# Performance work log

Measured on AMD Instinct MI355X. Metric: run time of the kernel, lower is better.

## Reference

```python
import jax, jax.numpy as jnp
import numpy as np

H = 128      # num_hidden
C = 384      # num_in
K = 32       # neighbors
N = 10000    # nodes
SCALE = 30.0
EPS = 1e-5

def _gelu(x):
    return jax.nn.gelu(x, approximate=False)  # torch GELU default is exact erf

def _ln(x, g, b):
    m = jnp.mean(x, axis=-1, keepdims=True)
    v = jnp.mean((x - m) ** 2, axis=-1, keepdims=True)
    return (x - m) * jax.lax.rsqrt(v + EPS) * g + b

def setup_inputs() -> dict:
    key = jax.random.key(0)
    ks = jax.random.split(key, 12)
    s = lambda fan_in: 1.0 / np.sqrt(fan_in)
    # weights stored [in, out] (transposed vs torch nn.Linear)
    return {
        "h_V": jax.random.normal(ks[0], (N, H), jnp.float32),
        "h_E": jax.random.normal(ks[1], (N, K, C), jnp.float32),
        "mask_V": jnp.ones((N,), jnp.float32),
        "mask_attend": jnp.ones((N, K), jnp.float32),
        "W1_w": jax.random.uniform(ks[2], (H + C, H), jnp.float32, -s(H + C), s(H + C)),
        "W1_b": jnp.zeros((H,), jnp.float32),
        "W2_w": jax.random.uniform(ks[3], (H, H), jnp.float32, -s(H), s(H)),
        "W2_b": jnp.zeros((H,), jnp.float32),
        "W3_w": jax.random.uniform(ks[4], (H, H), jnp.float32, -s(H), s(H)),
        "W3_b": jnp.zeros((H,), jnp.float32),
        "ln1_g": jnp.ones((H,), jnp.float32),
        "ln1_b": jnp.zeros((H,), jnp.float32),
        "Win_w": jax.random.uniform(ks[5], (H, 4 * H), jnp.float32, -s(H), s(H)),
        "Win_b": jnp.zeros((4 * H,), jnp.float32),
        "Wout_w": jax.random.uniform(ks[6], (4 * H, H), jnp.float32, -s(4 * H), s(4 * H)),
        "Wout_b": jnp.zeros((H,), jnp.float32),
        "ln2_g": jnp.ones((H,), jnp.float32),
        "ln2_b": jnp.zeros((H,), jnp.float32),
    }

def reference(h_V, h_E, mask_V, mask_attend,
              W1_w, W1_b, W2_w, W2_b, W3_w, W3_b,
              ln1_g, ln1_b, Win_w, Win_b, Wout_w, Wout_b, ln2_g, ln2_b):
    # expand node features along neighbor axis and concat with edge features
    h_V_expand = jnp.broadcast_to(h_V[:, None, :], (h_V.shape[0], h_E.shape[1], h_V.shape[1]))
    h_EV = jnp.concatenate([h_V_expand, h_E], axis=-1)          # [N, K, H+C]
    # per-edge 3-layer MLP message
    h = _gelu(h_EV @ W1_w + W1_b)                               # [N, K, H]
    h = _gelu(h @ W2_w + W2_b)
    h_message = h @ W3_w + W3_b
    h_message = mask_attend[..., None] * h_message
    dh = jnp.sum(h_message, axis=-2) / SCALE                    # [N, H]
    h_V = _ln(h_V + dh, ln1_g, ln1_b)
    # position-wise FFN
    dh = _gelu(h_V @ Win_w + Win_b) @ Wout_w + Wout_b
    h_V = _ln(h_V + dh, ln2_g, ln2_b)
    h_V = mask_V[:, None] * h_V
    return h_V
```

## Files before the change

### kernel.cpp

```cpp
#include <hip/hip_runtime.h>
#include <hip/hip_bf16.h>

#define NH 128
#define NC 384
#define NK 32

typedef __attribute__((ext_vector_type(8))) short short8v;
typedef __attribute__((ext_vector_type(4))) float f32x4;

#define MFMA16(a, b, c) __builtin_amdgcn_mfma_f32_16x16x32_bf16((a), (b), (c), 0, 0, 0)

__device__ __forceinline__ ushort f2bf(float x) {
  __hip_bfloat16 h = __float2bfloat16(x);
  ushort u;
  __builtin_memcpy(&u, &h, 2);
  return u;
}

__device__ __forceinline__ short8v ld8(const ushort* p) {
  return *reinterpret_cast<const short8v*>(p);
}
__device__ __forceinline__ void st8(ushort* p, short8v v) {
  *reinterpret_cast<short8v*>(p) = v;
}

__device__ __forceinline__ short8v pack8(float4 a, float4 b) {
  short8v v;
  v[0] = (short)f2bf(a.x); v[1] = (short)f2bf(a.y);
  v[2] = (short)f2bf(a.z); v[3] = (short)f2bf(a.w);
  v[4] = (short)f2bf(b.x); v[5] = (short)f2bf(b.y);
  v[6] = (short)f2bf(b.z); v[7] = (short)f2bf(b.w);
  return v;
}

__device__ __forceinline__ float gelu_f(float x) {
  float x2 = x * x;
  float m = __builtin_fmaf(0.07135481283f, x2, 1.595769122f);
  float e = __expf(-x * m);
  return x * __builtin_amdgcn_rcpf(1.0f + e);
}

__device__ __forceinline__ void gload_lds16(const float* g, float* l) {
  __builtin_amdgcn_global_load_lds(
      (const __attribute__((address_space(1))) unsigned int*)g,
      (__attribute__((address_space(3))) unsigned int*)l, 16, 0, 0);
}

__global__ __launch_bounds__(256) void pack_w(
    const float* __restrict__ W1, const float* __restrict__ W2,
    const float* __restrict__ W3, const float* __restrict__ Win,
    const float* __restrict__ Wout, ushort* __restrict__ ws) {
  int id = blockIdx.x * 256 + threadIdx.x;
  if (id < 65536) {
    int t = id, k = t >> 7, c = t & 127;
    ws[(((k >> 3) << 7) + c) * 8 + (k & 7)] = f2bf(W1[t]);
  } else if (id < 81920) {
    int t = id - 65536, k = t >> 7, c = t & 127;
    ws[65536 + (((k >> 3) << 7) + c) * 8 + (k & 7)] = f2bf(W2[t]);
  } else if (id < 98304) {
    int t = id - 81920, k = t >> 7, c = t & 127;
    ws[81920 + (((k >> 3) << 7) + c) * 8 + (k & 7)] = f2bf(W3[t]);
  } else if (id < 163840) {
    int t = id - 98304, k = t >> 9, c = t & 511;
    ws[98304 + (((k >> 3) << 9) + c) * 8 + (k & 7)] = f2bf(Win[t]);
  } else {
    int t = id - 163840, k = t >> 7, c = t & 127;
    ws[163840 + (((k >> 3) << 7) + c) * 8 + (k & 7)] = f2bf(Wout[t]);
  }
}


__device__ __forceinline__ void stage_issue(const float* __restrict__ hE,
    float* sF, int p, int chunk, int tid, int N) {
  const int w = tid >> 6, l = tid & 63;
#pragma unroll
  for (int j = 0; j < 4; ++j) {
    const int base16 = j * 512 + w * 64;
    const int fidx = (base16 + l) * 4;
    const int row = fidx >> 7;
    const int col = fidx & 127;
    const int node = row >> 5, e = row & 31;
    int n = 2 * p + node;
    if (n >= N) n = 0;
    const float* g = hE + ((size_t)n * NK + e) * NC + chunk * 128 + col;
    gload_lds16(g, sF + base16 * 4);
  }
}

__device__ __forceinline__ void convert_chunk(const float* sF, ushort* sB, int tid) {
#pragma unroll
  for (int j = 0; j < 4; ++j) {
    const int fi = j * 2048 + tid * 4;
    const float4 v = *reinterpret_cast<const float4*>(sF + fi);
    const int row = fi >> 7;
    const int col = fi & 127;
    const int c8 = col >> 3;
    ushort4 o;
    o.x = f2bf(v.x); o.y = f2bf(v.y); o.z = f2bf(v.z); o.w = f2bf(v.w);
    *reinterpret_cast<ushort4*>(sB + row * 128 + ((c8 ^ (row & 15)) << 3) + (col & 7)) = o;
  }
}

__device__ __forceinline__ void mfma_chunk(const ushort* __restrict__ buf,
    const ushort* __restrict__ Wp, int ktBase, f32x4 acc[4],
    int g, int lr, int colbase) {
#pragma unroll
  for (int j = 0; j < 4; ++j) {
    short8v b = ld8(Wp + (((ktBase + j) * 4 + g) * 128 + colbase) * 8);
    const int kcg = j * 4 + g;
#pragma unroll
    for (int rt = 0; rt < 4; ++rt) {
      const int row = rt * 16 + lr;
      short8v a = ld8(buf + row * 128 + ((kcg ^ (row & 15)) << 3));
      acc[rt] = MFMA16(a, b, acc[rt]);
    }
  }
}

__device__ __forceinline__ void epi_store(ushort* __restrict__ buf,
    const f32x4 acc[4], const float* __restrict__ bias, int colbase, int g) {
  const float bs = bias[colbase];
#pragma unroll
  for (int rt = 0; rt < 4; ++rt)
#pragma unroll
    for (int i = 0; i < 4; ++i) {
      const int rr = rt * 16 + g * 4 + i;
      buf[rr * 128 + ((((colbase >> 3) ^ (rr & 15)) << 3) | (colbase & 7))] =
          f2bf(gelu_f(acc[rt][i] + bs));
    }
}

__global__ __launch_bounds__(512, 4) void msg2(
    const float* __restrict__ hV, const float* __restrict__ hE,
    const float* __restrict__ mAtt, const ushort* __restrict__ wsu,
    const float* __restrict__ b1, const float* __restrict__ b2,
    const float* __restrict__ b3, const float* __restrict__ g1,
    const float* __restrict__ be1, float* __restrict__ hmidf,
    ushort* __restrict__ hmidb, int N) {
  const ushort* W1p = wsu;
  const ushort* W2p = wsu + 65536;
  const ushort* W3p = wsu + 81920;

  __shared__ float  sF[64 * 128];
  __shared__ ushort sB0[64 * 128];
  __shared__ ushort sB1[64 * 128];
  __shared__ ushort sHV[256];
  __shared__ float  sDh[256];
  __shared__ float  sRed[16];

  const int tid = threadIdx.x;
  const int w = tid >> 6, lane = tid & 63;
  const int g = lane >> 4, lr = lane & 15;
  const int colbase = (w << 4) + lr;
  const int p = blockIdx.x;

  stage_issue(hE, sF, p, 0, tid, N);
  if (tid < 32) {
    const int nd = tid >> 4, c8 = tid & 15;
    const int n = 2 * p + nd;
    const int ncl = n < N ? n : 0;
    const float4* hp = reinterpret_cast<const float4*>(hV + (size_t)ncl * NH + c8 * 8);
    st8(sHV + nd * 128 + c8 * 8, pack8(hp[0], hp[1]));
  }
  __syncthreads();

  convert_chunk(sF, sB0, tid);
  __syncthreads();

  stage_issue(hE, sF, p, 1, tid, N);

  f32x4 acc[4];
#pragma unroll
  for (int rt = 0; rt < 4; ++rt) acc[rt] = (f32x4){0.f, 0.f, 0.f, 0.f};

#pragma unroll
  for (int kt = 0; kt < 4; ++kt) {
    short8v bfr = ld8(W1p + ((kt * 4 + g) * 128 + colbase) * 8);
    short8v a0 = ld8(sHV + kt * 32 + g * 8);
    short8v a1 = ld8(sHV + 128 + kt * 32 + g * 8);
    acc[0] = MFMA16(a0, bfr, acc[0]);
    acc[1] = MFMA16(a0, bfr, acc[1]);
    acc[2] = MFMA16(a1, bfr, acc[2]);
    acc[3] = MFMA16(a1, bfr, acc[3]);
  }
  mfma_chunk(sB0, W1p, 4, acc, g, lr, colbase);
  __syncthreads();

  convert_chunk(sF, sB1, tid);
  __syncthreads();

  stage_issue(hE, sF, p, 2, tid, N);

  mfma_chunk(sB1, W1p, 8, acc, g, lr, colbase);
  __syncthreads();

  convert_chunk(sF, sB0, tid);
  __syncthreads();

  mfma_chunk(sB0, W1p, 12, acc, g, lr, colbase);
  epi_store(sB1, acc, b1, colbase, g);
  __syncthreads();

#pragma unroll
  for (int rt = 0; rt < 4; ++rt) acc[rt] = (f32x4){0.f, 0.f, 0.f, 0.f};
  mfma_chunk(sB1, W2p, 0, acc, g, lr, colbase);
  epi_store(sB0, acc, b2, colbase, g);
  __syncthreads();

#pragma unroll
  for (int rt = 0; rt < 4; ++rt) acc[rt] = (f32x4){0.f, 0.f, 0.f, 0.f};
  mfma_chunk(sB0, W3p, 0, acc, g, lr, colbase);
  {
    const float bias = b3[colbase];
    float ns0 = 0.f, ns1 = 0.f;
#pragma unroll
    for (int rt = 0; rt < 4; ++rt) {
      const int nd = rt >> 1;
      float s = 0.f;
#pragma unroll
      for (int i = 0; i < 4; ++i) {
        const int e2 = (rt & 1) * 16 + g * 4 + i;
        const float m =
            (2 * p + nd < N) ? mAtt[(size_t)(2 * p + nd) * NK + e2] : 0.f;
        s += (acc[rt][i] + bias) * m;
      }
      s += __shfl_xor(s, 16, 64);
      s += __shfl_xor(s, 32, 64);
      if (rt < 2) ns0 += s; else ns1 += s;
    }
    if (g == 0) { sDh[colbase] = ns0; sDh[128 + colbase] = ns1; }
  }
  __syncthreads();

  float x_ln = 0.f;
  if (tid < 256) {
    const int nd = tid >> 7, i = tid & 127;
    const int gn = 2 * p + nd;
    if (gn < N)
      x_ln = hV[(size_t)gn * NH + i] + sDh[nd * NH + i] * (1.f / 30.f);
    float s = x_ln, qv = x_ln * x_ln;
#pragma unroll
    for (int d = 1; d < 64; d <<= 1) {
      s += __shfl_xor(s, d, 64);
      qv += __shfl_xor(qv, d, 64);
    }
    if (lane == 0) { sRed[w * 2] = s; sRed[w * 2 + 1] = qv; }
  }
  __syncthreads();
  if (tid < 256) {
    const int nd = tid >> 7, i = tid & 127;
    const int gn = 2 * p + nd;
    if (gn < N) {
      const int wb = nd * 2;
      const float s = sRed[wb * 2] + sRed[wb * 2 + 2];
      const float qv = sRed[wb * 2 + 1] + sRed[wb * 2 + 3];
      const float mean = s * (1.f / 128.f);
      const float var = qv * (1.f / 128.f) - mean * mean;
      const float y = (x_ln - mean) * rsqrtf(var + 1e-5f) * g1[i] + be1[i];
      hmidf[(size_t)gn * NH + i] = y;
      hmidb[(size_t)gn * NH + i] = f2bf(y);
    }
  }
}

__global__ __launch_bounds__(256, 4) void ffn_kernel(
    const ushort* __restrict__ wsu, const float* __restrict__ binf,
    const float* __restrict__ boutf, const float* __restrict__ g2,
    const float* __restrict__ be2, const float* __restrict__ maskV,
    const float* __restrict__ hmidf, const ushort* __restrict__ hmidb,
    float* __restrict__ out, int N) {
  const ushort* Winp = wsu + 98304;
  const ushort* Woutp = wsu + 163840;

  __shared__ ushort sX[16 * 128];
  __shared__ ushort sHf[16 * 512];
  __shared__ float  sY[16 * 132];

  const int tid = threadIdx.x;
  const int w = tid >> 6, lane = tid & 63;
  const int g = lane >> 4, lr = lane & 15;
  const int n0 = blockIdx.x * 16;

  {
    const int rr = tid >> 4, c8 = tid & 15;
    const int n = n0 + rr;
    short8v v = {0, 0, 0, 0, 0, 0, 0, 0};
    if (n < N) v = ld8(hmidb + (size_t)n * NH + c8 * 8);
    st8(sX + rr * 128 + ((c8 ^ (rr & 15)) << 3), v);
  }
  __syncthreads();

#pragma unroll
  for (int ct8 = 0; ct8 < 8; ++ct8) {
    const int col = (w * 8 + ct8) * 16 + lr;
    f32x4 a0acc = (f32x4){0.f, 0.f, 0.f, 0.f};
#pragma unroll
    for (int kt = 0; kt < 4; ++kt) {
      short8v b = ld8(Winp + ((kt * 4 + g) * 512 + col) * 8);
      const int kcg = kt * 4 + g;
      const int r0 = lr;
      short8v a0 = ld8(sX + r0 * 128 + ((kcg ^ (r0 & 15)) << 3));
      a0acc = MFMA16(a0, b, a0acc);
    }
    const float bi = binf[col];
#pragma unroll
    for (int i = 0; i < 4; ++i) {
      const int rr = g * 4 + i;
      const float v0 = gelu_f(a0acc[i] + bi);
      sHf[rr * 512 + ((((col >> 3) ^ (rr & 15)) << 3) | (col & 7))] = f2bf(v0);
    }
  }
  __syncthreads();

  f32x4 o0 = (f32x4){0.f, 0.f, 0.f, 0.f}, o1 = o0;
#pragma unroll
  for (int kt = 0; kt < 16; ++kt) {
    const int kcg = kt * 4 + g;
    const int c0 = (2 * w) * 16 + lr, c1 = (2 * w + 1) * 16 + lr;
    short8v b0 = ld8(Woutp + (kcg * 128 + c0) * 8);
    short8v b1 = ld8(Woutp + (kcg * 128 + c1) * 8);
    const int r0 = lr;
    short8v a0 = ld8(sHf + r0 * 512 + ((kcg ^ (r0 & 15)) << 3));
    o0 = MFMA16(a0, b0, o0);
    o1 = MFMA16(a0, b1, o1);
  }
#pragma unroll
  for (int ct = 0; ct < 2; ++ct) {
    const int col = (2 * w + ct) * 16 + lr;
    const float bo = boutf[col];
    const f32x4 oo = ct ? o1 : o0;
#pragma unroll
    for (int i = 0; i < 4; ++i) {
      const int rr = g * 4 + i;
      const int n = n0 + rr;
      const float resid = (n < N) ? hmidf[(size_t)n * NH + col] : 0.f;
      sY[rr * 132 + col] = oo[i] + bo + resid;
    }
  }
  __syncthreads();

  {
    const int rr = tid >> 4, qq = tid & 15;
    const int n = n0 + rr;
    float vals[8];
    float s = 0.f, qs = 0.f;
    const float* yr = sY + rr * 132 + qq * 8;
#pragma unroll
    for (int j = 0; j < 8; ++j) { float x = yr[j]; vals[j] = x; s += x; qs += x * x; }
    s += __shfl_xor(s, 1, 64);  qs += __shfl_xor(qs, 1, 64);
    s += __shfl_xor(s, 2, 64);  qs += __shfl_xor(qs, 2, 64);
    s += __shfl_xor(s, 4, 64);  qs += __shfl_xor(qs, 4, 64);
    s += __shfl_xor(s, 8, 64);  qs += __shfl_xor(qs, 8, 64);
    const float mean = s * (1.f / 128.f);
    const float var = qs * (1.f / 128.f) - mean * mean;
    const float rs = rsqrtf(var + 1e-5f);
    if (n < N) {
      const float mv = maskV[n];
#pragma unroll
      for (int j = 0; j < 8; ++j) {
        const int col = qq * 8 + j;
        out[(size_t)n * NH + col] = ((vals[j] - mean) * rs * g2[col] + be2[col]) * mv;
      }
    }
  }
}

extern "C" void kernel_launch(void* const* d_in, const int* in_sizes, int n_in,
                              void* d_out, int out_size, void* d_ws, size_t ws_size,
                              hipStream_t stream) {
  const float* hV   = (const float*)d_in[0];
  const float* hE   = (const float*)d_in[1];
  const float* mV   = (const float*)d_in[2];
  const float* mAtt = (const float*)d_in[3];
  const float* W1   = (const float*)d_in[4];
  const float* b1   = (const float*)d_in[5];
  const float* W2   = (const float*)d_in[6];
  const float* b2   = (const float*)d_in[7];
  const float* W3   = (const float*)d_in[8];
  const float* b3   = (const float*)d_in[9];
  const float* g1   = (const float*)d_in[10];
  const float* be1  = (const float*)d_in[11];
  const float* Win  = (const float*)d_in[12];
  const float* binf = (const float*)d_in[13];
  const float* Wout = (const float*)d_in[14];
  const float* bout = (const float*)d_in[15];
  const float* g2   = (const float*)d_in[16];
  const float* be2  = (const float*)d_in[17];

  const int N = in_sizes[0] / NH;

  ushort* wsu = (ushort*)d_ws;
  float*  hmidf = (float*)((char*)d_ws + 458752);
  ushort* hmidb = (ushort*)((char*)d_ws + 458752 + (size_t)N * NH * 4);

  pack_w<<<896, 256, 0, stream>>>(W1, W2, W3, Win, Wout, wsu);

  const int pairs = (N + 1) / 2;
  msg2<<<pairs, 512, 0, stream>>>(hV, hE, mAtt, wsu, b1, b2, b3, g1, be1,
                                  hmidf, hmidb, N);
  ffn_kernel<<<(N + 15) / 16, 256, 0, stream>>>(wsu, binf, bout, g2, be2, mV,
                                                hmidf, hmidb, (float*)d_out, N);
  (void)n_in; (void)out_size; (void)ws_size;
}
```

Before: 184.0 us.

## Stream edge features through registers with 64-column double-buffered LDS chunks

Replaces the global_load_lds staging of h_E into a float LDS buffer, followed by a separate convert pass, with direct per-thread float4 register loads. Each 64-column chunk is converted to bf16 straight into one of two swizzled LDS buffers, with two chunks of loads kept in flight. The main K loop becomes six smaller chunks with one barrier each instead of several syncthreads per 128-column chunk. This removes the fp32 LDS buffer, which lowers LDS use, and cuts LDS round trips. In exchange it needs more registers for the in-flight loads, and the added barriers could limit how well loads overlap with MFMA work.

```diff
diff --git a/kernel.cpp b/kernel.cpp
--- a/kernel.cpp
+++ b/kernel.cpp
@@ -40,10 +40,10 @@
   return x * __builtin_amdgcn_rcpf(1.0f + e);
 }
 
-__device__ __forceinline__ void gload_lds16(const float* g, float* l) {
-  __builtin_amdgcn_global_load_lds(
-      (const __attribute__((address_space(1))) unsigned int*)g,
-      (__attribute__((address_space(3))) unsigned int*)l, 16, 0, 0);
+__device__ __forceinline__ void lds_barrier() {
+  asm volatile("s_waitcnt lgkmcnt(0)" ::: "memory");
+  __builtin_amdgcn_sched_barrier(0);
+  __builtin_amdgcn_s_barrier();
 }
 
 __global__ __launch_bounds__(256) void pack_w(
@@ -70,67 +70,72 @@
 }
 
 
-__device__ __forceinline__ void stage_issue(const float* __restrict__ hE,
-    float* sF, int p, int chunk, int tid, int N) {
-  const int w = tid >> 6, l = tid & 63;
-#pragma unroll
-  for (int j = 0; j < 4; ++j) {
-    const int base16 = j * 512 + w * 64;
-    const int fidx = (base16 + l) * 4;
-    const int row = fidx >> 7;
-    const int col = fidx & 127;
-    const int node = row >> 5, e = row & 31;
-    int n = 2 * p + node;
-    if (n >= N) n = 0;
-    const float* g = hE + ((size_t)n * NK + e) * NC + chunk * 128 + col;
-    gload_lds16(g, sF + base16 * 4);
-  }
-}
-
-__device__ __forceinline__ void convert_chunk(const float* sF, ushort* sB, int tid) {
-#pragma unroll
-  for (int j = 0; j < 4; ++j) {
-    const int fi = j * 2048 + tid * 4;
-    const float4 v = *reinterpret_cast<const float4*>(sF + fi);
-    const int row = fi >> 7;
-    const int col = fi & 127;
-    const int c8 = col >> 3;
-    ushort4 o;
-    o.x = f2bf(v.x); o.y = f2bf(v.y); o.z = f2bf(v.z); o.w = f2bf(v.w);
-    *reinterpret_cast<ushort4*>(sB + row * 128 + ((c8 ^ (row & 15)) << 3) + (col & 7)) = o;
+__device__ __forceinline__ void issue_chunk(const float* __restrict__ hE,
+    int p, int c, int tid, int N, float4& a, float4& b) {
+  const int r = tid >> 3;
+  const int cb = (tid & 7) * 8;
+  const int node = r >> 5, e = r & 31;
+  int n = 2 * p + node;
+  if (n >= N) n = 0;
+  const float* g = hE + ((size_t)n * NK + e) * NC + c * 64 + cb;
+  const float4* gp = reinterpret_cast<const float4*>(g);
+  a = gp[0];
+  b = gp[1];
+}
+
+__device__ __forceinline__ void convert_regs(ushort* __restrict__ sC, int tid,
+    float4 a, float4 b, bool zz) {
+  const int r = tid >> 3, cg = tid & 7;
+  short8v v = zz ? (short8v){0, 0, 0, 0, 0, 0, 0, 0} : pack8(a, b);
+  st8(sC + r * 64 + ((cg ^ (r & 7)) << 3), v);
+}
+
+__device__ __forceinline__ void mfma_chunk64(const ushort* __restrict__ sC,
+    const ushort* __restrict__ W1p, int j, f32x4 acc[4],
+    int g, int lr, int outcol) {
+#pragma unroll
+  for (int jj = 0; jj < 2; ++jj) {
+    short8v bfr = ld8(W1p + (((16 + j * 8 + jj * 4 + g) * 128) + outcol) * 8);
+    const int akg = jj * 4 + g;
+#pragma unroll
+    for (int rt = 0; rt < 4; ++rt) {
+      const int row = rt * 16 + lr;
+      short8v af = ld8(sC + row * 64 + ((akg ^ (row & 7)) << 3));
+      acc[rt] = MFMA16(af, bfr, acc[rt]);
+    }
   }
 }
 
 __device__ __forceinline__ void mfma_chunk(const ushort* __restrict__ buf,
     const ushort* __restrict__ Wp, int ktBase, f32x4 acc[4],
-    int g, int lr, int colbase) {
+    int g, int lr, int outcol) {
 #pragma unroll
   for (int j = 0; j < 4; ++j) {
-    short8v b = ld8(Wp + (((ktBase + j) * 4 + g) * 128 + colbase) * 8);
+    short8v bfr = ld8(Wp + (((ktBase + j) * 4 + g) * 128 + outcol) * 8);
     const int kcg = j * 4 + g;
 #pragma unroll
     for (int rt = 0; rt < 4; ++rt) {
       const int row = rt * 16 + lr;
-      short8v a = ld8(buf + row * 128 + ((kcg ^ (row & 15)) << 3));
-      acc[rt] = MFMA16(a, b, acc[rt]);
+      short8v af = ld8(buf + row * 128 + ((kcg ^ (row & 15)) << 3));
+      acc[rt] = MFMA16(af, bfr, acc[rt]);
     }
   }
 }
 
 __device__ __forceinline__ void epi_store(ushort* __restrict__ buf,
-    const f32x4 acc[4], const float* __restrict__ bias, int colbase, int g) {
-  const float bs = bias[colbase];
+    const f32x4 acc[4], const float* __restrict__ bias, int outcol, int g) {
+  const float bs = bias[outcol];
 #pragma unroll
   for (int rt = 0; rt < 4; ++rt)
 #pragma unroll
     for (int i = 0; i < 4; ++i) {
       const int rr = rt * 16 + g * 4 + i;
-      buf[rr * 128 + ((((colbase >> 3) ^ (rr & 15)) << 3) | (colbase & 7))] =
+      buf[rr * 128 + ((((outcol >> 3) ^ (rr & 15)) << 3) | (outcol & 7))] =
           f2bf(gelu_f(acc[rt][i] + bs));
     }
 }
 
-__global__ __launch_bounds__(512, 4) void msg2(
+__global__ __launch_bounds__(512, 4) void msg3(
     const float* __restrict__ hV, const float* __restrict__ hE,
     const float* __restrict__ mAtt, const ushort* __restrict__ wsu,
     const float* __restrict__ b1, const float* __restrict__ b2,
@@ -141,9 +146,8 @@
   const ushort* W2p = wsu + 65536;
   const ushort* W3p = wsu + 81920;
 
-  __shared__ float  sF[64 * 128];
-  __shared__ ushort sB0[64 * 128];
-  __shared__ ushort sB1[64 * 128];
+  __shared__ ushort sC[2][4096];
+  __shared__ ushort sH2[8192];
   __shared__ ushort sHV[256];
   __shared__ float  sDh[256];
   __shared__ float  sRed[16];
@@ -151,10 +155,14 @@
   const int tid = threadIdx.x;
   const int w = tid >> 6, lane = tid & 63;
   const int g = lane >> 4, lr = lane & 15;
-  const int colbase = (w << 4) + lr;
+  const int outcol = (w << 4) + lr;
   const int p = blockIdx.x;
-
-  stage_issue(hE, sF, p, 0, tid, N);
+  const bool zz = (2 * p + ((tid >> 3) >> 5)) >= N;
+
+  float4 eA, eB, oA, oB;
+
+  issue_chunk(hE, p, 0, tid, N, eA, eB);
+  issue_chunk(hE, p, 1, tid, N, oA, oB);
   if (tid < 32) {
     const int nd = tid >> 4, c8 = tid & 15;
     const int n = 2 * p + nd;
@@ -162,12 +170,8 @@
     const float4* hp = reinterpret_cast<const float4*>(hV + (size_t)ncl * NH + c8 * 8);
     st8(sHV + nd * 128 + c8 * 8, pack8(hp[0], hp[1]));
   }
-  __syncthreads();
-
-  convert_chunk(sF, sB0, tid);
-  __syncthreads();
-
-  stage_issue(hE, sF, p, 1, tid, N);
+  convert_regs(sC[0], tid, eA, eB, zz);
+  lds_barrier();
 
   f32x4 acc[4];
 #pragma unroll
@@ -175,7 +179,7 @@
 
 #pragma unroll
   for (int kt = 0; kt < 4; ++kt) {
-    short8v bfr = ld8(W1p + ((kt * 4 + g) * 128 + colbase) * 8);
+    short8v bfr = ld8(W1p + ((kt * 4 + g) * 128 + outcol) * 8);
     short8v a0 = ld8(sHV + kt * 32 + g * 8);
     short8v a1 = ld8(sHV + 128 + kt * 32 + g * 8);
     acc[0] = MFMA16(a0, bfr, acc[0]);
@@ -183,35 +187,44 @@
     acc[2] = MFMA16(a1, bfr, acc[2]);
     acc[3] = MFMA16(a1, bfr, acc[3]);
   }
-  mfma_chunk(sB0, W1p, 4, acc, g, lr, colbase);
-  __syncthreads();
-
-  convert_chunk(sF, sB1, tid);
-  __syncthreads();
-
-  stage_issue(hE, sF, p, 2, tid, N);
-
-  mfma_chunk(sB1, W1p, 8, acc, g, lr, colbase);
-  __syncthreads();
-
-  convert_chunk(sF, sB0, tid);
-  __syncthreads();
-
-  mfma_chunk(sB0, W1p, 12, acc, g, lr, colbase);
-  epi_store(sB1, acc, b1, colbase, g);
+
+  issue_chunk(hE, p, 2, tid, N, eA, eB);
+  mfma_chunk64(sC[0], W1p, 0, acc, g, lr, outcol);
+  convert_regs(sC[1], tid, oA, oB, zz);
+  lds_barrier();
+  issue_chunk(hE, p, 3, tid, N, oA, oB);
+  mfma_chunk64(sC[1], W1p, 1, acc, g, lr, outcol);
+  convert_regs(sC[0], tid, eA, eB, zz);
+  lds_barrier();
+  issue_chunk(hE, p, 4, tid, N, eA, eB);
+  mfma_chunk64(sC[0], W1p, 2, acc, g, lr, outcol);
+  convert_regs(sC[1], tid, oA, oB, zz);
+  lds_barrier();
+  issue_chunk(hE, p, 5, tid, N, oA, oB);
+  mfma_chunk64(sC[1], W1p, 3, acc, g, lr, outcol);
+  convert_regs(sC[0], tid, eA, eB, zz);
+  lds_barrier();
+  mfma_chunk64(sC[0], W1p, 4, acc, g, lr, outcol);
+  convert_regs(sC[1], tid, oA, oB, zz);
+  lds_barrier();
+  mfma_chunk64(sC[1], W1p, 5, acc, g, lr, outcol);
+  __syncthreads();
+
+  ushort* sH1 = &sC[0][0];
+  epi_store(sH1, acc, b1, outcol, g);
   __syncthreads();
 
 #pragma unroll
   for (int rt = 0; rt < 4; ++rt) acc[rt] = (f32x4){0.f, 0.f, 0.f, 0.f};
-  mfma_chunk(sB1, W2p, 0, acc, g, lr, colbase);
-  epi_store(sB0, acc, b2, colbase, g);
+  mfma_chunk(sH1, W2p, 0, acc, g, lr, outcol);
+  epi_store(sH2, acc, b2, outcol, g);
   __syncthreads();
 
 #pragma unroll
   for (int rt = 0; rt < 4; ++rt) acc[rt] = (f32x4){0.f, 0.f, 0.f, 0.f};
-  mfma_chunk(sB0, W3p, 0, acc, g, lr, colbase);
+  mfma_chunk(sH2, W3p, 0, acc, g, lr, outcol);
   {
-    const float bias = b3[colbase];
+    const float bias = b3[outcol];
     float ns0 = 0.f, ns1 = 0.f;
 #pragma unroll
     for (int rt = 0; rt < 4; ++rt) {
@@ -228,7 +241,7 @@
       s += __shfl_xor(s, 32, 64);
       if (rt < 2) ns0 += s; else ns1 += s;
     }
-    if (g == 0) { sDh[colbase] = ns0; sDh[128 + colbase] = ns1; }
+    if (g == 0) { sDh[outcol] = ns0; sDh[128 + outcol] = ns1; }
   }
   __syncthreads();
 
@@ -396,7 +409,7 @@
   pack_w<<<896, 256, 0, stream>>>(W1, W2, W3, Win, Wout, wsu);
 
   const int pairs = (N + 1) / 2;
-  msg2<<<pairs, 512, 0, stream>>>(hV, hE, mAtt, wsu, b1, b2, b3, g1, be1,
+  msg3<<<pairs, 512, 0, stream>>>(hV, hE, mAtt, wsu, b1, b2, b3, g1, be1,
                                   hmidf, hmidb, N);
   ffn_kernel<<<(N + 15) / 16, 256, 0, stream>>>(wsu, binf, bout, g2, be2, mV,
                                                 hmidf, hmidb, (float*)d_out, N);
```

After: 168.0 us. 8.7% less time.
